# Performance work log

Hardware: AMD Instinct MI355X
Metric: run time of the kernel (lower is better)

Reference implementation:

```python
import jax, jax.numpy as jnp
import numpy as np
from math import factorial

# ---- static configuration (matches init_kwargs) ----
IRREPS_IN1 = [(32, 0, 1), (32, 1, -1), (32, 2, 1)]   # (mul, l, parity)
IRREPS_SH  = [(1, 0, 1), (1, 1, -1), (1, 2, 1)]
IRREPS_OUT = [(32, 0, 1), (32, 1, -1), (32, 2, 1)]
NUM_BASIS = 10
HIDDEN = 16
CUTOFF = 4.0
P_ENV = 6  # dimenet envelope_exponent (5) + 1

# ---- real Wigner 3j (Clebsch-Gordan in real SH basis), computed once in numpy ----
def _su2_cg(j1, j2, j3, m1, m2, m3):
    if m3 != m1 + m2:
        return 0.0
    f = factorial
    vmin = max(-j1 + j2 + m3, -j1 + m1, 0)
    vmax = min(j2 + j3 + m1, j3 - j1 + j2, j3 + m3)
    c = (f(2*j3+1) * f(j3+j1-j2) * f(j3-j1+j2) * f(j1+j2-j3) / f(j1+j2+j3+1)
         * f(j3+m3) * f(j3-m3) / (f(j1+m1) * f(j1-m1) * f(j2+m2) * f(j2-m2))) ** 0.5
    s = 0.0
    for v in range(vmin, vmax + 1):
        s += (-1)**(v + j2 + m2) * f(j2+j3+m1-v) * f(j1-m1+v) / (
             f(v) * f(j3-j1+j2-v) * f(j3+m3-v) * f(v+j1-j2-m3))
    return c * s

def _q(l):  # real -> complex SH change of basis
    q = np.zeros((2*l+1, 2*l+1), dtype=complex)
    for m in range(-l, 0):
        q[l+m, l+abs(m)] = 2**-0.5
        q[l+m, l-abs(m)] = -1j * 2**-0.5
    q[l, l] = 1.0
    for m in range(1, l+1):
        q[l+m, l+abs(m)] = (-1)**m * 2**-0.5
        q[l+m, l-abs(m)] = 1j * (-1)**m * 2**-0.5
    return (-1j)**l * q

def _wigner_3j(l1, l2, l3):
    csu2 = np.array([[[ _su2_cg(l1, l2, l3, m1, m2, m3)
                       for m3 in range(-l3, l3+1)]
                      for m2 in range(-l2, l2+1)]
                     for m1 in range(-l1, l1+1)], dtype=complex)
    c = np.einsum('ij,kl,mn,ikm->jln', _q(l1), _q(l2), np.conj(_q(l3)), csu2)
    c = np.real(c)
    n = np.linalg.norm(c)
    return c / n if n > 0 else c

def _slices(irreps):
    s, off = [], 0
    for mul, l, p in irreps:
        d = mul * (2*l + 1)
        s.append((off, off + d))
        off += d
    return s, off

SL1, DIM_IN1 = _slices(IRREPS_IN1)
SL2, DIM_SH = _slices(IRREPS_SH)
SL3, DIM_OUT = _slices(IRREPS_OUT)

_raw = []
for i1, (m1, l1, p1) in enumerate(IRREPS_IN1):
    for i2, (m2, l2, p2) in enumerate(IRREPS_SH):
        for i3, (m3, l3, p3) in enumerate(IRREPS_OUT):
            if p1 * p2 == p3 and abs(l1 - l2) <= l3 <= l1 + l2:
                _raw.append((i1, i2, i3))

_fan = {}
for i1, i2, i3 in _raw:  # path_normalization='element': fan-in per output slot
    _fan[i3] = _fan.get(i3, 0) + IRREPS_IN1[i1][0] * IRREPS_SH[i2][0]

INSTR = []
WEIGHT_NUMEL = 0
for i1, i2, i3 in _raw:
    m1, l1, _ = IRREPS_IN1[i1]
    m2, l2, _ = IRREPS_SH[i2]
    m3, l3, _ = IRREPS_OUT[i3]
    pw = ((2*l3 + 1) / _fan[i3]) ** 0.5  # irrep_normalization='component'
    C = _wigner_3j(l1, l2, l3).astype(np.float32)
    INSTR.append((i1, i2, i3, m1, l1, m2, l2, m3, l3, WEIGHT_NUMEL, pw, C))
    WEIGHT_NUMEL += m1 * m2 * m3

# ---- radial network: Bessel basis (with dimenet envelope) -> Linear -> SiLU -> Linear ----
def _radial(distance, freq, W1, b1, W2, b2):
    d = distance[:, 0]                      # squeeze(-1) -> [E]
    x = (d / CUTOFF)[:, None]               # [E, 1]
    p = P_ENV
    a = -(p + 1) * (p + 2) / 2.0
    b = float(p * (p + 2))
    c = -p * (p + 1) / 2.0
    env = (1.0 / x + a * x**(p-1) + b * x**p + c * x**(p+1)) * (x < 1.0).astype(x.dtype)
    basis = env * jnp.sin(freq * x)         # [E, NUM_BASIS]
    h = jax.nn.silu(basis @ W1 + b1)
    return h @ W2 + b2                      # [E, WEIGHT_NUMEL]

# ---- fully connected tensor product (uvw, external per-edge weights) ----
def _tp(x, sh, weights):
    E = x.shape[0]
    acc = [jnp.zeros((E, m, 2*l + 1), x.dtype) for m, l, _ in IRREPS_OUT]
    for (i1, i2, i3, m1, l1, m2, l2, m3, l3, woff, pw, C) in INSTR:
        a, b = SL1[i1]; xb = x[:, a:b].reshape(E, m1, 2*l1 + 1)
        a, b = SL2[i2]; sb = sh[:, a:b].reshape(E, m2, 2*l2 + 1)
        w = weights[:, woff:woff + m1*m2*m3].reshape(E, m1, m2, m3)
        Cj = jnp.asarray(C)
        acc[i3] = acc[i3] + pw * jnp.einsum('euvw,ijk,eui,evj->ewk', w, Cj, xb, sb)
    return jnp.concatenate([a.reshape(E, -1) for a in acc], axis=1)


def setup_inputs() -> dict:
    key = jax.random.key(0)
    ks = jax.random.split(key, 6)
    E = 16384
    x = jax.random.normal(ks[0], (E, DIM_IN1), jnp.float32)
    rel_pos_sh = jax.random.normal(ks[1], (E, DIM_SH), jnp.float32)
    # distances strictly inside (0, cutoff) so envelope 1/x and mask are benign
    distance = 0.25 + 3.5 * jax.random.uniform(ks[2], (E, 1), jnp.float32)
    freq = jnp.pi * jnp.arange(1, NUM_BASIS + 1, dtype=jnp.float32)
    W1 = 0.4 * jax.random.normal(ks[3], (NUM_BASIS, HIDDEN), jnp.float32)
    b1 = jnp.zeros((HIDDEN,), jnp.float32)
    W2 = 0.1 * jax.random.normal(ks[4], (HIDDEN, WEIGHT_NUMEL), jnp.float32)
    b2 = jnp.zeros((WEIGHT_NUMEL,), jnp.float32)
    return {"x": x, "rel_pos_sh": rel_pos_sh, "distance": distance,
            "freq": freq, "W1": W1, "b1": b1, "W2": W2, "b2": b2}


def reference(x, rel_pos_sh, distance, freq, W1, b1, W2, b2):
    weights = _radial(distance, freq, W1, b1, W2, b2)
    return _tp(x, rel_pos_sh, weights)
```

## Files before the change

kernel.cpp:

```cpp
#include <hip/hip_runtime.h>
#include <cmath>
#include <complex>
#include <cstring>
#include <algorithm>

#define DIM_IN  288
#define DIM_SHD 9
#define NB      10
#define NH      16
#define EPB     16
#define BLOCK   256
#define NINSTR  11
#define XSTR    292
#define ZG_STRIDE 116
#define ZG_SIZE  (16 * ZG_STRIDE)
#define W2B_ELEMS (NINSTR * 32 * 32 * 32)

#define OFF_SH 7424
#define POOLSZ 7616

typedef __attribute__((ext_vector_type(8))) short  short8b;
typedef __attribute__((ext_vector_type(4))) float  f32x4;
typedef __attribute__((ext_vector_type(2))) float  f32x2;

__device__ float g_C[NINSTR][125];

__device__ __forceinline__ unsigned short f2bf(float f) {
  unsigned int u = __float_as_uint(f);
  unsigned int r = (u + 0x7fffu + ((u >> 16) & 1u)) >> 16;
  return (unsigned short)r;
}

__global__ __launch_bounds__(256) void prep_w2(const float* __restrict__ W2,
                                               const float* __restrict__ b2,
                                               unsigned short* __restrict__ W2b) {
  int gid = blockIdx.x * 256 + threadIdx.x;
  if (gid < W2B_ELEMS) {
    int c = gid >> 5, t = gid & 31;
    float v = (t < 16) ? W2[(size_t)t * 11264 + c] : (t == 16 ? b2[c] : 0.0f);
    W2b[gid] = f2bf(v);
  }
}

template<int INS,int D1,int D2,int D3,int OFF2,int SLOT>
__device__ __forceinline__ void z_one(const float (&xv)[D1],
                                      const float* __restrict__ she,
                                      float* __restrict__ zo)
{
  const float* __restrict__ Cp = g_C[INS];
  constexpr int NP = D3 / 2;
  f32x2 zk2[NP > 0 ? NP : 1];
  float zkl = 0.f;
  #pragma unroll
  for (int m = 0; m < NP; ++m) zk2[m] = (f32x2){0.f, 0.f};
  #pragma unroll
  for (int i = 0; i < D1; ++i) {
    #pragma unroll
    for (int j = 0; j < D2; ++j) {
      float pr = xv[i] * she[OFF2 + j];
      f32x2 pr2 = {pr, pr};
      const float* cb = Cp + (i * D2 + j) * D3;
      #pragma unroll
      for (int m = 0; m < NP; ++m) {
        f32x2 cc = {cb[2 * m], cb[2 * m + 1]};
        zk2[m] = __builtin_elementwise_fma(cc, pr2, zk2[m]);
      }
      zkl = fmaf(cb[D3 - 1], pr, zkl);
    }
  }
  #pragma unroll
  for (int m = 0; m < NP; ++m) {
    zo[(SLOT + 2 * m) * 8]     = zk2[m].x;
    zo[(SLOT + 2 * m + 1) * 8] = zk2[m].y;
  }
  zo[(SLOT + D3 - 1) * 8] = zkl;
}

template<int D1,int OFF1>
__device__ __forceinline__ void load_x(const float* __restrict__ xg, int e0,
                                       int e, int u, float (&xv)[D1]) {
  const float* xp = xg + (size_t)(e0 + e) * DIM_IN + OFF1 + u * D1;
  #pragma unroll
  for (int i = 0; i < D1; ++i) xv[i] = xp[i];
}

__device__ __forceinline__ void z_group_l0(int lane, int q, int e0,
    const float* __restrict__ xg, const float* __restrict__ s_sh,
    float* __restrict__ zw) {
  #pragma unroll
  for (int s = 0; s < 2; ++s) {
    int id = lane + s * 64;
    int e = id >> 3, ul = id & 7, u = q * 8 + ul;
    float xv[1];
    load_x<1, 0>(xg, e0, e, u, xv);
    const float* she = s_sh + e * 12;
    float* zo = zw + e * ZG_STRIDE + ul;
    z_one<0, 1, 1, 1, 0, 0>(xv, she, zo);
    z_one<1, 1, 3, 3, 1, 1>(xv, she, zo);
    z_one<2, 1, 5, 5, 4, 4>(xv, she, zo);
  }
}

__device__ __forceinline__ void z_group_l1(int lane, int q, int e0,
    const float* __restrict__ xg, const float* __restrict__ s_sh,
    float* __restrict__ zw) {
  #pragma unroll
  for (int s = 0; s < 2; ++s) {
    int id = lane + s * 64;
    int e = id >> 3, ul = id & 7, u = q * 8 + ul;
    float xv[3];
    load_x<3, 32>(xg, e0, e, u, xv);
    const float* she = s_sh + e * 12;
    float* zo = zw + e * ZG_STRIDE + ul;
    z_one<3, 3, 1, 3, 0, 0>(xv, she, zo);
    z_one<4, 3, 3, 1, 1, 3>(xv, she, zo);
    z_one<5, 3, 3, 5, 1, 4>(xv, she, zo);
    z_one<6, 3, 5, 3, 4, 9>(xv, she, zo);
  }
}

__device__ __forceinline__ void z_group_l2(int lane, int q, int e0,
    const float* __restrict__ xg, const float* __restrict__ s_sh,
    float* __restrict__ zw) {
  #pragma unroll
  for (int s = 0; s < 2; ++s) {
    int id = lane + s * 64;
    int e = id >> 3, ul = id & 7, u = q * 8 + ul;
    float xv[5];
    load_x<5, 128>(xg, e0, e, u, xv);
    const float* she = s_sh + e * 12;
    float* zo = zw + e * ZG_STRIDE + ul;
    z_one< 7, 5, 1, 5, 0, 0>(xv, she, zo);
    z_one< 8, 5, 3, 3, 1, 5>(xv, she, zo);
    z_one< 9, 5, 5, 1, 4, 8>(xv, she, zo);
    z_one<10, 5, 5, 5, 4, 9>(xv, she, zo);
  }
}

template<int INS,int D3,int SB,int SLOT>
__device__ __forceinline__ void contract_q(
    int ls, int lq, int q,
    const unsigned short* __restrict__ W2b,
    const float* __restrict__ zw, short8b hB, f32x2 (&acc)[2][2][9])
{
  const unsigned short* Ap =
      W2b + ((size_t)(INS * 32 + q * 8) * 32 + ls) * 32 + lq * 8;
  const float* zb = zw + ls * ZG_STRIDE + SLOT * 8;
  const f32x4 zero4 = {0.f, 0.f, 0.f, 0.f};

  short8b R0c = *(const short8b*)(Ap);
  short8b R1c = *(const short8b*)(Ap + 512);
  short8b R0n = *(const short8b*)(Ap + 1024);
  short8b R1n = *(const short8b*)(Ap + 1536);
  f32x4 w0_cur = __builtin_amdgcn_mfma_f32_16x16x32_bf16(R0c, hB, zero4, 0, 0, 0);
  f32x4 w1_cur = __builtin_amdgcn_mfma_f32_16x16x32_bf16(R1c, hB, zero4, 0, 0, 0);

  #pragma unroll
  for (int c = 0; c < 2; ++c) {
    float4 zq[D3];
    #pragma unroll
    for (int k = 0; k < D3; ++k)
      zq[k] = *(const float4*)(zb + k * 8 + c * 4);
    #pragma unroll
    for (int i = 0; i < 4; ++i) {
      const int g = c * 4 + i;
      f32x4 w0n, w1n;
      if (g < 7) {
        w0n = __builtin_amdgcn_mfma_f32_16x16x32_bf16(R0n, hB, zero4, 0, 0, 0);
        w1n = __builtin_amdgcn_mfma_f32_16x16x32_bf16(R1n, hB, zero4, 0, 0, 0);
        if (g + 2 < 8) {
          R0n = *(const short8b*)(Ap + (size_t)(g + 2) * 1024);
          R1n = *(const short8b*)(Ap + (size_t)(g + 2) * 1024 + 512);
        }
      }
      f32x2 w0lo = {w0_cur[0], w0_cur[1]};
      f32x2 w0hi = {w0_cur[2], w0_cur[3]};
      f32x2 w1lo = {w1_cur[0], w1_cur[1]};
      f32x2 w1hi = {w1_cur[2], w1_cur[3]};
      #pragma unroll
      for (int k = 0; k < D3; ++k) {
        const float zz = (i == 0) ? zq[k].x : (i == 1) ? zq[k].y
                       : (i == 2) ? zq[k].z : zq[k].w;
        f32x2 zv = {zz, zz};
        acc[0][0][SB + k] = __builtin_elementwise_fma(w0lo, zv, acc[0][0][SB + k]);
        acc[0][1][SB + k] = __builtin_elementwise_fma(w0hi, zv, acc[0][1][SB + k]);
        acc[1][0][SB + k] = __builtin_elementwise_fma(w1lo, zv, acc[1][0][SB + k]);
        acc[1][1][SB + k] = __builtin_elementwise_fma(w1hi, zv, acc[1][1][SB + k]);
      }
      if (g < 7) { w0_cur = w0n; w1_cur = w1n; }
    }
  }
}

__global__ __launch_bounds__(BLOCK, 2) void conv_kernel(
    const float* __restrict__ xg, const float* __restrict__ shg,
    const float* __restrict__ dist, const float* __restrict__ freq,
    const float* __restrict__ W1, const float* __restrict__ b1,
    const unsigned short* __restrict__ W2b,
    float* __restrict__ out)
{
  __shared__ float s_pool[POOLSZ];
  float* s_sh = s_pool + OFF_SH;

  const int tid = threadIdx.x;
  const int e0 = blockIdx.x * EPB;
  const int lane = tid & 63;
  const int ls = lane & 15;
  const int lq = lane >> 4;
  const int q   = tid >> 6;
  float* zw = s_pool + q * ZG_SIZE;
  float* s_basis = s_pool + 2 * ZG_SIZE;
  unsigned short* s_hb = (unsigned short*)(s_pool + 3 * ZG_SIZE);

  if (tid < EPB * DIM_SHD) {
    int e = tid / DIM_SHD, c = tid - (tid / DIM_SHD) * DIM_SHD;
    s_sh[e * 12 + c] = shg[(size_t)(e0 + e) * DIM_SHD + c];
  }
  if (tid < EPB * NB) {
    int e = tid / NB, n = tid - (tid / NB) * NB;
    float d  = dist[e0 + e];
    float xv = d * 0.25f;
    float x2 = xv * xv, x4 = x2 * x2, x5 = x4 * xv;
    float env = 1.0f / xv + x5 * fmaf(xv, fmaf(xv, -21.0f, 48.0f), -28.0f);
    env = (xv < 1.0f) ? env : 0.0f;
    s_basis[e * NB + n] = env * sinf(freq[n] * xv);
  }
  __syncthreads();

  {
    int e = tid >> 4, t = tid & 15;
    float v = b1[t];
    #pragma unroll
    for (int n = 0; n < NB; ++n) v = fmaf(s_basis[e * NB + n], W1[n * NH + t], v);
    v = v / (1.0f + expf(-v));
    s_hb[e * 32 + t] = f2bf(v);
    s_hb[e * 32 + t + 16] = (t == 0) ? (unsigned short)0x3F80 : (unsigned short)0;
  }
  __syncthreads();
  short8b hB = *(const short8b*)(s_hb + ls * 32 + lq * 8);
  __syncthreads();

  f32x2 acc[2][2][9];
  #pragma unroll
  for (int wt = 0; wt < 2; ++wt)
    #pragma unroll
    for (int p = 0; p < 2; ++p)
      #pragma unroll
      for (int a = 0; a < 9; ++a) acc[wt][p][a] = (f32x2){0.f, 0.f};

  z_group_l0(lane, q, e0, xg, s_sh, zw);
  contract_q< 0, 1, 0, 0>(ls, lq, q, W2b, zw, hB, acc);
  contract_q< 1, 3, 1, 1>(ls, lq, q, W2b, zw, hB, acc);
  contract_q< 2, 5, 4, 4>(ls, lq, q, W2b, zw, hB, acc);

  z_group_l1(lane, q, e0, xg, s_sh, zw);
  contract_q< 3, 3, 1, 0>(ls, lq, q, W2b, zw, hB, acc);
  contract_q< 4, 1, 0, 3>(ls, lq, q, W2b, zw, hB, acc);
  contract_q< 5, 5, 4, 4>(ls, lq, q, W2b, zw, hB, acc);
  contract_q< 6, 3, 1, 9>(ls, lq, q, W2b, zw, hB, acc);

  z_group_l2(lane, q, e0, xg, s_sh, zw);
  contract_q< 7, 5, 4, 0>(ls, lq, q, W2b, zw, hB, acc);
  contract_q< 8, 3, 1, 5>(ls, lq, q, W2b, zw, hB, acc);
  contract_q< 9, 1, 0, 8>(ls, lq, q, W2b, zw, hB, acc);
  contract_q<10, 5, 4, 9>(ls, lq, q, W2b, zw, hB, acc);

  __syncthreads();
  float* s_og = s_pool;
  #pragma unroll
  for (int ph = 3; ph >= 0; --ph) {
    if (q == ph) {
      float* row = s_og + ls * XSTR;
      #pragma unroll
      for (int wt = 0; wt < 2; ++wt) {
        #pragma unroll
        for (int r = 0; r < 4; ++r) {
          const int w = wt * 16 + lq * 4 + r;
          float vals[9];
          #pragma unroll
          for (int a = 0; a < 9; ++a)
            vals[a] = (r & 1) ? acc[wt][r >> 1][a].y : acc[wt][r >> 1][a].x;
          if (ph == 3) {
            row[w] = vals[0];
            #pragma unroll
            for (int k = 0; k < 3; ++k) row[32 + w * 3 + k] = vals[1 + k];
            #pragma unroll
            for (int k = 0; k < 5; ++k) row[128 + w * 5 + k] = vals[4 + k];
          } else {
            row[w] += vals[0];
            #pragma unroll
            for (int k = 0; k < 3; ++k) row[32 + w * 3 + k] += vals[1 + k];
            #pragma unroll
            for (int k = 0; k < 5; ++k) row[128 + w * 5 + k] += vals[4 + k];
          }
        }
      }
    }
    __syncthreads();
  }
  for (int i4 = tid; i4 < EPB * 72; i4 += BLOCK) {
    int e = i4 / 72, r = i4 - e * 72;
    float4 v = *(const float4*)(s_og + e * XSTR + r * 4);
    *(float4*)(out + (size_t)(e0 + e) * DIM_IN + r * 4) = v;
  }
}

typedef std::complex<double> cd;

static double factd(int n) { double r = 1; for (int i = 2; i <= n; ++i) r *= i; return r; }

static double su2_cg(int j1, int j2, int j3, int m1, int m2, int m3) {
  if (m3 != m1 + m2) return 0.0;
  int vmin = std::max(std::max(-j1 + j2 + m3, -j1 + m1), 0);
  int vmax = std::min(std::min(j2 + j3 + m1, j3 - j1 + j2), j3 + m3);
  if (vmax < vmin) return 0.0;
  double c = std::sqrt(
      factd(2*j3+1) * factd(j3+j1-j2) * factd(j3-j1+j2) * factd(j1+j2-j3) / factd(j1+j2+j3+1)
      * factd(j3+m3) * factd(j3-m3)
      / (factd(j1+m1) * factd(j1-m1) * factd(j2+m2) * factd(j2-m2)));
  double s = 0.0;
  for (int v = vmin; v <= vmax; ++v) {
    double sg = ((v + j2 + m2) & 1) ? -1.0 : 1.0;
    s += sg * factd(j2+j3+m1-v) * factd(j1-m1+v)
         / (factd(v) * factd(j3-j1+j2-v) * factd(j3+m3-v) * factd(v+j1-j2-m3));
  }
  return c * s;
}

static void qmat(int l, cd q[5][5]) {
  for (int a = 0; a < 5; ++a) for (int b = 0; b < 5; ++b) q[a][b] = cd(0, 0);
  const double s = 1.0 / std::sqrt(2.0);
  for (int m = -l; m < 0; ++m) {
    q[l + m][l - m] = cd(s, 0);
    q[l + m][l + m] = cd(0, -s);
  }
  q[l][l] = cd(1, 0);
  for (int m = 1; m <= l; ++m) {
    double sg = (m & 1) ? -1.0 : 1.0;
    q[l + m][l + m] = cd(sg * s, 0);
    q[l + m][l - m] = cd(0, sg * s);
  }
  cd ph = (l == 0) ? cd(1, 0) : (l == 1) ? cd(0, -1) : cd(-1, 0);
  for (int a = 0; a < 5; ++a) for (int b = 0; b < 5; ++b) q[a][b] *= ph;
}

static void wigner3j(int l1, int l2, int l3, double C[5][5][5]) {
  int d1 = 2*l1+1, d2 = 2*l2+1, d3 = 2*l3+1;
  cd q1[5][5], q2[5][5], q3[5][5];
  qmat(l1, q1); qmat(l2, q2); qmat(l3, q3);
  double norm2 = 0;
  for (int j = 0; j < d1; ++j)
    for (int l = 0; l < d2; ++l)
      for (int n = 0; n < d3; ++n) {
        cd sum(0, 0);
        for (int i = 0; i < d1; ++i)
          for (int k = 0; k < d2; ++k)
            for (int m = 0; m < d3; ++m) {
              double cg = su2_cg(l1, l2, l3, i - l1, k - l2, m - l3);
              if (cg != 0.0) sum += q1[i][j] * q2[k][l] * std::conj(q3[m][n]) * cg;
            }
        C[j][l][n] = sum.real();
        norm2 += C[j][l][n] * C[j][l][n];
      }
  double nrm = std::sqrt(norm2);
  if (nrm > 0)
    for (int j = 0; j < d1; ++j)
      for (int l = 0; l < d2; ++l)
        for (int n = 0; n < d3; ++n) C[j][l][n] /= nrm;
}

static void build_C_host(float C_out[NINSTR][125]) {
  const int L1[NINSTR] = {0,0,0,1,1,1,1,2,2,2,2};
  const int L2[NINSTR] = {0,1,2,0,1,1,2,0,1,2,2};
  const int L3[NINSTR] = {0,1,2,1,0,2,1,2,1,0,2};
  std::memset(C_out, 0, sizeof(float) * NINSTR * 125);
  for (int ins = 0; ins < NINSTR; ++ins) {
    int l1 = L1[ins], l2 = L2[ins], l3 = L3[ins];
    int d1 = 2*l1+1, d2 = 2*l2+1, d3 = 2*l3+1;
    double C[5][5][5];
    wigner3j(l1, l2, l3, C);
    double fan = (l3 == 0) ? 96.0 : 128.0;
    double pw = std::sqrt((2*l3+1) / fan);
    for (int i = 0; i < d1; ++i)
      for (int j = 0; j < d2; ++j)
        for (int k = 0; k < d3; ++k)
          C_out[ins][(i * d2 + j) * d3 + k] = (float)(pw * C[i][j][k]);
  }
}

extern "C" void kernel_launch(void* const* d_in, const int* in_sizes, int n_in,
                              void* d_out, int out_size, void* d_ws, size_t ws_size,
                              hipStream_t stream) {
  static float hC[NINSTR][125];
  build_C_host(hC);
  void* dC = nullptr;
  hipGetSymbolAddress(&dC, HIP_SYMBOL(g_C));
  hipMemcpyAsync(dC, hC, sizeof(hC), hipMemcpyHostToDevice, stream);

  const float* xg   = (const float*)d_in[0];
  const float* shg  = (const float*)d_in[1];
  const float* dist = (const float*)d_in[2];
  const float* freq = (const float*)d_in[3];
  const float* W1   = (const float*)d_in[4];
  const float* b1   = (const float*)d_in[5];
  const float* W2   = (const float*)d_in[6];
  const float* b2   = (const float*)d_in[7];
  float* out = (float*)d_out;
  unsigned short* W2b = (unsigned short*)d_ws;

  prep_w2<<<(W2B_ELEMS + 255) / 256, 256, 0, stream>>>(W2, b2, W2b);

  int E = in_sizes[2];
  int blocks = E / EPB;
  conv_kernel<<<blocks, BLOCK, 0, stream>>>(xg, shg, dist, freq, W1, b1, W2b, out);
}
```

Before: 68.27 us.

## Split u-dimension across eight waves per block instead of four

```diff
diff --git a/kernel.cpp b/kernel.cpp
--- a/kernel.cpp
+++ b/kernel.cpp
@@ -9,11 +9,11 @@
 #define NB      10
 #define NH      16
 #define EPB     16
-#define BLOCK   256
+#define BLOCK   512
 #define NINSTR  11
 #define XSTR    292
-#define ZG_STRIDE 116
-#define ZG_SIZE  (16 * ZG_STRIDE)
+#define ZW_STRIDE 58
+#define ZW_SIZE  (16 * ZW_STRIDE)
 #define W2B_ELEMS (NINSTR * 32 * 32 * 32)
 
 #define OFF_SH 7424
@@ -70,10 +70,10 @@
   }
   #pragma unroll
   for (int m = 0; m < NP; ++m) {
-    zo[(SLOT + 2 * m) * 8]     = zk2[m].x;
-    zo[(SLOT + 2 * m + 1) * 8] = zk2[m].y;
-  }
-  zo[(SLOT + D3 - 1) * 8] = zkl;
+    zo[(SLOT + 2 * m) * 4]     = zk2[m].x;
+    zo[(SLOT + 2 * m + 1) * 4] = zk2[m].y;
+  }
+  zo[(SLOT + D3 - 1) * 4] = zkl;
 }
 
 template<int D1,int OFF1>
@@ -84,110 +84,88 @@
   for (int i = 0; i < D1; ++i) xv[i] = xp[i];
 }
 
-__device__ __forceinline__ void z_group_l0(int lane, int q, int e0,
+__device__ __forceinline__ void z_group_l0(int lane, int q8, int e0,
     const float* __restrict__ xg, const float* __restrict__ s_sh,
     float* __restrict__ zw) {
-  #pragma unroll
-  for (int s = 0; s < 2; ++s) {
-    int id = lane + s * 64;
-    int e = id >> 3, ul = id & 7, u = q * 8 + ul;
-    float xv[1];
-    load_x<1, 0>(xg, e0, e, u, xv);
-    const float* she = s_sh + e * 12;
-    float* zo = zw + e * ZG_STRIDE + ul;
-    z_one<0, 1, 1, 1, 0, 0>(xv, she, zo);
-    z_one<1, 1, 3, 3, 1, 1>(xv, she, zo);
-    z_one<2, 1, 5, 5, 4, 4>(xv, she, zo);
-  }
-}
-
-__device__ __forceinline__ void z_group_l1(int lane, int q, int e0,
+  int e = lane >> 2, ul = lane & 3, u = q8 * 4 + ul;
+  float xv[1];
+  load_x<1, 0>(xg, e0, e, u, xv);
+  const float* she = s_sh + e * 12;
+  float* zo = zw + e * ZW_STRIDE + ul;
+  z_one<0, 1, 1, 1, 0, 0>(xv, she, zo);
+  z_one<1, 1, 3, 3, 1, 1>(xv, she, zo);
+  z_one<2, 1, 5, 5, 4, 4>(xv, she, zo);
+}
+
+__device__ __forceinline__ void z_group_l1(int lane, int q8, int e0,
     const float* __restrict__ xg, const float* __restrict__ s_sh,
     float* __restrict__ zw) {
-  #pragma unroll
-  for (int s = 0; s < 2; ++s) {
-    int id = lane + s * 64;
-    int e = id >> 3, ul = id & 7, u = q * 8 + ul;
-    float xv[3];
-    load_x<3, 32>(xg, e0, e, u, xv);
-    const float* she = s_sh + e * 12;
-    float* zo = zw + e * ZG_STRIDE + ul;
-    z_one<3, 3, 1, 3, 0, 0>(xv, she, zo);
-    z_one<4, 3, 3, 1, 1, 3>(xv, she, zo);
-    z_one<5, 3, 3, 5, 1, 4>(xv, she, zo);
-    z_one<6, 3, 5, 3, 4, 9>(xv, she, zo);
-  }
-}
-
-__device__ __forceinline__ void z_group_l2(int lane, int q, int e0,
+  int e = lane >> 2, ul = lane & 3, u = q8 * 4 + ul;
+  float xv[3];
+  load_x<3, 32>(xg, e0, e, u, xv);
+  const float* she = s_sh + e * 12;
+  float* zo = zw + e * ZW_STRIDE + ul;
+  z_one<3, 3, 1, 3, 0, 0>(xv, she, zo);
+  z_one<4, 3, 3, 1, 1, 3>(xv, she, zo);
+  z_one<5, 3, 3, 5, 1, 4>(xv, she, zo);
+  z_one<6, 3, 5, 3, 4, 9>(xv, she, zo);
+}
+
+__device__ __forceinline__ void z_group_l2(int lane, int q8, int e0,
     const float* __restrict__ xg, const float* __restrict__ s_sh,
     float* __restrict__ zw) {
-  #pragma unroll
-  for (int s = 0; s < 2; ++s) {
-    int id = lane + s * 64;
-    int e = id >> 3, ul = id & 7, u = q * 8 + ul;
-    float xv[5];
-    load_x<5, 128>(xg, e0, e, u, xv);
-    const float* she = s_sh + e * 12;
-    float* zo = zw + e * ZG_STRIDE + ul;
-    z_one< 7, 5, 1, 5, 0, 0>(xv, she, zo);
-    z_one< 8, 5, 3, 3, 1, 5>(xv, she, zo);
-    z_one< 9, 5, 5, 1, 4, 8>(xv, she, zo);
-    z_one<10, 5, 5, 5, 4, 9>(xv, she, zo);
-  }
+  int e = lane >> 2, ul = lane & 3, u = q8 * 4 + ul;
+  float xv[5];
+  load_x<5, 128>(xg, e0, e, u, xv);
+  const float* she = s_sh + e * 12;
+  float* zo = zw + e * ZW_STRIDE + ul;
+  z_one< 7, 5, 1, 5, 0, 0>(xv, she, zo);
+  z_one< 8, 5, 3, 3, 1, 5>(xv, she, zo);
+  z_one< 9, 5, 5, 1, 4, 8>(xv, she, zo);
+  z_one<10, 5, 5, 5, 4, 9>(xv, she, zo);
 }
 
 template<int INS,int D3,int SB,int SLOT>
-__device__ __forceinline__ void contract_q(
-    int ls, int lq, int q,
+__device__ __forceinline__ void contract8(
+    int ls, int lq, int q8,
     const unsigned short* __restrict__ W2b,
     const float* __restrict__ zw, short8b hB, f32x2 (&acc)[2][2][9])
 {
   const unsigned short* Ap =
-      W2b + ((size_t)(INS * 32 + q * 8) * 32 + ls) * 32 + lq * 8;
-  const float* zb = zw + ls * ZG_STRIDE + SLOT * 8;
+      W2b + ((size_t)(INS * 32 + q8 * 4) * 32 + ls) * 32 + lq * 8;
+  const float* zb = zw + ls * ZW_STRIDE + SLOT * 4;
   const f32x4 zero4 = {0.f, 0.f, 0.f, 0.f};
 
-  short8b R0c = *(const short8b*)(Ap);
-  short8b R1c = *(const short8b*)(Ap + 512);
-  short8b R0n = *(const short8b*)(Ap + 1024);
-  short8b R1n = *(const short8b*)(Ap + 1536);
-  f32x4 w0_cur = __builtin_amdgcn_mfma_f32_16x16x32_bf16(R0c, hB, zero4, 0, 0, 0);
-  f32x4 w1_cur = __builtin_amdgcn_mfma_f32_16x16x32_bf16(R1c, hB, zero4, 0, 0, 0);
-
-  #pragma unroll
-  for (int c = 0; c < 2; ++c) {
-    float4 zq[D3];
+  #pragma unroll
+  for (int wt = 0; wt < 2; ++wt) {
+    const unsigned short* Aw = Ap + wt * 512;
+    short8b A0 = *(const short8b*)(Aw);
+    short8b A1 = *(const short8b*)(Aw + 1024);
+    short8b A2 = *(const short8b*)(Aw + 2048);
+    short8b A3 = *(const short8b*)(Aw + 3072);
+    f32x4 w_cur = __builtin_amdgcn_mfma_f32_16x16x32_bf16(A0, hB, zero4, 0, 0, 0);
+    f32x2 zp[D3];
     #pragma unroll
-    for (int k = 0; k < D3; ++k)
-      zq[k] = *(const float4*)(zb + k * 8 + c * 4);
-    #pragma unroll
-    for (int i = 0; i < 4; ++i) {
-      const int g = c * 4 + i;
-      f32x4 w0n, w1n;
-      if (g < 7) {
-        w0n = __builtin_amdgcn_mfma_f32_16x16x32_bf16(R0n, hB, zero4, 0, 0, 0);
-        w1n = __builtin_amdgcn_mfma_f32_16x16x32_bf16(R1n, hB, zero4, 0, 0, 0);
-        if (g + 2 < 8) {
-          R0n = *(const short8b*)(Ap + (size_t)(g + 2) * 1024);
-          R1n = *(const short8b*)(Ap + (size_t)(g + 2) * 1024 + 512);
-        }
-      }
-      f32x2 w0lo = {w0_cur[0], w0_cur[1]};
-      f32x2 w0hi = {w0_cur[2], w0_cur[3]};
-      f32x2 w1lo = {w1_cur[0], w1_cur[1]};
-      f32x2 w1hi = {w1_cur[2], w1_cur[3]};
+    for (int g = 0; g < 4; ++g) {
+      f32x4 w_next;
+      if (g == 0) w_next = __builtin_amdgcn_mfma_f32_16x16x32_bf16(A1, hB, zero4, 0, 0, 0);
+      if (g == 1) w_next = __builtin_amdgcn_mfma_f32_16x16x32_bf16(A2, hB, zero4, 0, 0, 0);
+      if (g == 2) w_next = __builtin_amdgcn_mfma_f32_16x16x32_bf16(A3, hB, zero4, 0, 0, 0);
+      if ((g & 1) == 0) {
+        #pragma unroll
+        for (int k = 0; k < D3; ++k)
+          zp[k] = *(const f32x2*)(zb + k * 4 + g);
+      }
+      f32x2 wlo = {w_cur[0], w_cur[1]};
+      f32x2 whi = {w_cur[2], w_cur[3]};
       #pragma unroll
       for (int k = 0; k < D3; ++k) {
-        const float zz = (i == 0) ? zq[k].x : (i == 1) ? zq[k].y
-                       : (i == 2) ? zq[k].z : zq[k].w;
+        const float zz = (g & 1) ? zp[k].y : zp[k].x;
         f32x2 zv = {zz, zz};
-        acc[0][0][SB + k] = __builtin_elementwise_fma(w0lo, zv, acc[0][0][SB + k]);
-        acc[0][1][SB + k] = __builtin_elementwise_fma(w0hi, zv, acc[0][1][SB + k]);
-        acc[1][0][SB + k] = __builtin_elementwise_fma(w1lo, zv, acc[1][0][SB + k]);
-        acc[1][1][SB + k] = __builtin_elementwise_fma(w1hi, zv, acc[1][1][SB + k]);
-      }
-      if (g < 7) { w0_cur = w0n; w1_cur = w1n; }
+        acc[wt][0][SB + k] = __builtin_elementwise_fma(wlo, zv, acc[wt][0][SB + k]);
+        acc[wt][1][SB + k] = __builtin_elementwise_fma(whi, zv, acc[wt][1][SB + k]);
+      }
+      if (g < 3) w_cur = w_next;
     }
   }
 }
@@ -207,10 +185,10 @@
   const int lane = tid & 63;
   const int ls = lane & 15;
   const int lq = lane >> 4;
-  const int q   = tid >> 6;
-  float* zw = s_pool + q * ZG_SIZE;
-  float* s_basis = s_pool + 2 * ZG_SIZE;
-  unsigned short* s_hb = (unsigned short*)(s_pool + 3 * ZG_SIZE);
+  const int q8  = tid >> 6;
+  float* zw = s_pool + q8 * ZW_SIZE;
+  float* s_basis = s_pool + 6 * ZW_SIZE;
+  unsigned short* s_hb = (unsigned short*)(s_pool + 7 * ZW_SIZE);
 
   if (tid < EPB * DIM_SHD) {
     int e = tid / DIM_SHD, c = tid - (tid / DIM_SHD) * DIM_SHD;
@@ -227,7 +205,7 @@
   }
   __syncthreads();
 
-  {
+  if (tid < EPB * NH) {
     int e = tid >> 4, t = tid & 15;
     float v = b1[t];
     #pragma unroll
@@ -248,28 +226,28 @@
       #pragma unroll
       for (int a = 0; a < 9; ++a) acc[wt][p][a] = (f32x2){0.f, 0.f};
 
-  z_group_l0(lane, q, e0, xg, s_sh, zw);
-  contract_q< 0, 1, 0, 0>(ls, lq, q, W2b, zw, hB, acc);
-  contract_q< 1, 3, 1, 1>(ls, lq, q, W2b, zw, hB, acc);
-  contract_q< 2, 5, 4, 4>(ls, lq, q, W2b, zw, hB, acc);
-
-  z_group_l1(lane, q, e0, xg, s_sh, zw);
-  contract_q< 3, 3, 1, 0>(ls, lq, q, W2b, zw, hB, acc);
-  contract_q< 4, 1, 0, 3>(ls, lq, q, W2b, zw, hB, acc);
-  contract_q< 5, 5, 4, 4>(ls, lq, q, W2b, zw, hB, acc);
-  contract_q< 6, 3, 1, 9>(ls, lq, q, W2b, zw, hB, acc);
-
-  z_group_l2(lane, q, e0, xg, s_sh, zw);
-  contract_q< 7, 5, 4, 0>(ls, lq, q, W2b, zw, hB, acc);
-  contract_q< 8, 3, 1, 5>(ls, lq, q, W2b, zw, hB, acc);
-  contract_q< 9, 1, 0, 8>(ls, lq, q, W2b, zw, hB, acc);
-  contract_q<10, 5, 4, 9>(ls, lq, q, W2b, zw, hB, acc);
+  z_group_l0(lane, q8, e0, xg, s_sh, zw);
+  contract8< 0, 1, 0, 0>(ls, lq, q8, W2b, zw, hB, acc);
+  contract8< 1, 3, 1, 1>(ls, lq, q8, W2b, zw, hB, acc);
+  contract8< 2, 5, 4, 4>(ls, lq, q8, W2b, zw, hB, acc);
+
+  z_group_l1(lane, q8, e0, xg, s_sh, zw);
+  contract8< 3, 3, 1, 0>(ls, lq, q8, W2b, zw, hB, acc);
+  contract8< 4, 1, 0, 3>(ls, lq, q8, W2b, zw, hB, acc);
+  contract8< 5, 5, 4, 4>(ls, lq, q8, W2b, zw, hB, acc);
+  contract8< 6, 3, 1, 9>(ls, lq, q8, W2b, zw, hB, acc);
+
+  z_group_l2(lane, q8, e0, xg, s_sh, zw);
+  contract8< 7, 5, 4, 0>(ls, lq, q8, W2b, zw, hB, acc);
+  contract8< 8, 3, 1, 5>(ls, lq, q8, W2b, zw, hB, acc);
+  contract8< 9, 1, 0, 8>(ls, lq, q8, W2b, zw, hB, acc);
+  contract8<10, 5, 4, 9>(ls, lq, q8, W2b, zw, hB, acc);
 
   __syncthreads();
   float* s_og = s_pool;
   #pragma unroll
-  for (int ph = 3; ph >= 0; --ph) {
-    if (q == ph) {
+  for (int ph = 7; ph >= 0; --ph) {
+    if (q8 == ph) {
       float* row = s_og + ls * XSTR;
       #pragma unroll
       for (int wt = 0; wt < 2; ++wt) {
@@ -280,7 +258,7 @@
           #pragma unroll
           for (int a = 0; a < 9; ++a)
             vals[a] = (r & 1) ? acc[wt][r >> 1][a].y : acc[wt][r >> 1][a].x;
-          if (ph == 3) {
+          if (ph == 7) {
             row[w] = vals[0];
             #pragma unroll
             for (int k = 0; k < 3; ++k) row[32 + w * 3 + k] = vals[1 + k];
```

Result: slower. 102.7 us (+50.5%).

## Split output-channel halves into two sequential passes to halve accumulator registers

Applied to the files above, without the earlier changes.

```diff
diff --git a/kernel.cpp b/kernel.cpp
--- a/kernel.cpp
+++ b/kernel.cpp
@@ -137,23 +137,20 @@
   }
 }
 
-template<int INS,int D3,int SB,int SLOT>
-__device__ __forceinline__ void contract_q(
+template<int INS,int D3,int SB,int SLOT,int WT>
+__device__ __forceinline__ void contract_h(
     int ls, int lq, int q,
     const unsigned short* __restrict__ W2b,
-    const float* __restrict__ zw, short8b hB, f32x2 (&acc)[2][2][9])
+    const float* __restrict__ zw, short8b hB, f32x2 (&acc)[2][9])
 {
   const unsigned short* Ap =
-      W2b + ((size_t)(INS * 32 + q * 8) * 32 + ls) * 32 + lq * 8;
+      W2b + ((size_t)(INS * 32 + q * 8) * 32 + ls) * 32 + lq * 8 + WT * 512;
   const float* zb = zw + ls * ZG_STRIDE + SLOT * 8;
   const f32x4 zero4 = {0.f, 0.f, 0.f, 0.f};
 
-  short8b R0c = *(const short8b*)(Ap);
-  short8b R1c = *(const short8b*)(Ap + 512);
-  short8b R0n = *(const short8b*)(Ap + 1024);
-  short8b R1n = *(const short8b*)(Ap + 1536);
-  f32x4 w0_cur = __builtin_amdgcn_mfma_f32_16x16x32_bf16(R0c, hB, zero4, 0, 0, 0);
-  f32x4 w1_cur = __builtin_amdgcn_mfma_f32_16x16x32_bf16(R1c, hB, zero4, 0, 0, 0);
+  short8b Rc = *(const short8b*)(Ap);
+  short8b Rn = *(const short8b*)(Ap + 1024);
+  f32x4 w_cur = __builtin_amdgcn_mfma_f32_16x16x32_bf16(Rc, hB, zero4, 0, 0, 0);
 
   #pragma unroll
   for (int c = 0; c < 2; ++c) {
@@ -164,32 +161,96 @@
     #pragma unroll
     for (int i = 0; i < 4; ++i) {
       const int g = c * 4 + i;
-      f32x4 w0n, w1n;
+      f32x4 w_next;
       if (g < 7) {
-        w0n = __builtin_amdgcn_mfma_f32_16x16x32_bf16(R0n, hB, zero4, 0, 0, 0);
-        w1n = __builtin_amdgcn_mfma_f32_16x16x32_bf16(R1n, hB, zero4, 0, 0, 0);
-        if (g + 2 < 8) {
-          R0n = *(const short8b*)(Ap + (size_t)(g + 2) * 1024);
-          R1n = *(const short8b*)(Ap + (size_t)(g + 2) * 1024 + 512);
-        }
+        w_next = __builtin_amdgcn_mfma_f32_16x16x32_bf16(Rn, hB, zero4, 0, 0, 0);
+        if (g + 2 < 8) Rn = *(const short8b*)(Ap + (size_t)(g + 2) * 1024);
       }
-      f32x2 w0lo = {w0_cur[0], w0_cur[1]};
-      f32x2 w0hi = {w0_cur[2], w0_cur[3]};
-      f32x2 w1lo = {w1_cur[0], w1_cur[1]};
-      f32x2 w1hi = {w1_cur[2], w1_cur[3]};
+      f32x2 wlo = {w_cur[0], w_cur[1]};
+      f32x2 whi = {w_cur[2], w_cur[3]};
       #pragma unroll
       for (int k = 0; k < D3; ++k) {
         const float zz = (i == 0) ? zq[k].x : (i == 1) ? zq[k].y
                        : (i == 2) ? zq[k].z : zq[k].w;
         f32x2 zv = {zz, zz};
-        acc[0][0][SB + k] = __builtin_elementwise_fma(w0lo, zv, acc[0][0][SB + k]);
-        acc[0][1][SB + k] = __builtin_elementwise_fma(w0hi, zv, acc[0][1][SB + k]);
-        acc[1][0][SB + k] = __builtin_elementwise_fma(w1lo, zv, acc[1][0][SB + k]);
-        acc[1][1][SB + k] = __builtin_elementwise_fma(w1hi, zv, acc[1][1][SB + k]);
+        acc[0][SB + k] = __builtin_elementwise_fma(wlo, zv, acc[0][SB + k]);
+        acc[1][SB + k] = __builtin_elementwise_fma(whi, zv, acc[1][SB + k]);
       }
-      if (g < 7) { w0_cur = w0n; w1_cur = w1n; }
+      if (g < 7) w_cur = w_next;
     }
   }
+}
+
+template<int WT>
+__device__ __forceinline__ void run_pass(
+    int tid, int lane, int ls, int lq, int q, int e0,
+    const float* __restrict__ xg, const float* __restrict__ s_sh,
+    float* __restrict__ zw, float* __restrict__ s_pool,
+    const unsigned short* __restrict__ W2b, short8b hB,
+    float* __restrict__ out)
+{
+  f32x2 acc[2][9];
+  #pragma unroll
+  for (int p = 0; p < 2; ++p)
+    #pragma unroll
+    for (int a = 0; a < 9; ++a) acc[p][a] = (f32x2){0.f, 0.f};
+
+  z_group_l0(lane, q, e0, xg, s_sh, zw);
+  contract_h< 0, 1, 0, 0, WT>(ls, lq, q, W2b, zw, hB, acc);
+  contract_h< 1, 3, 1, 1, WT>(ls, lq, q, W2b, zw, hB, acc);
+  contract_h< 2, 5, 4, 4, WT>(ls, lq, q, W2b, zw, hB, acc);
+
+  z_group_l1(lane, q, e0, xg, s_sh, zw);
+  contract_h< 3, 3, 1, 0, WT>(ls, lq, q, W2b, zw, hB, acc);
+  contract_h< 4, 1, 0, 3, WT>(ls, lq, q, W2b, zw, hB, acc);
+  contract_h< 5, 5, 4, 4, WT>(ls, lq, q, W2b, zw, hB, acc);
+  contract_h< 6, 3, 1, 9, WT>(ls, lq, q, W2b, zw, hB, acc);
+
+  z_group_l2(lane, q, e0, xg, s_sh, zw);
+  contract_h< 7, 5, 4, 0, WT>(ls, lq, q, W2b, zw, hB, acc);
+  contract_h< 8, 3, 1, 5, WT>(ls, lq, q, W2b, zw, hB, acc);
+  contract_h< 9, 1, 0, 8, WT>(ls, lq, q, W2b, zw, hB, acc);
+  contract_h<10, 5, 4, 9, WT>(ls, lq, q, W2b, zw, hB, acc);
+
+  __syncthreads();
+  float* s_og = s_pool;
+  #pragma unroll
+  for (int ph = 3; ph >= 0; --ph) {
+    if (q == ph) {
+      float* row = s_og + ls * XSTR;
+      #pragma unroll
+      for (int r = 0; r < 4; ++r) {
+        const int w = WT * 16 + lq * 4 + r;
+        float vals[9];
+        #pragma unroll
+        for (int a = 0; a < 9; ++a)
+          vals[a] = (r & 1) ? acc[r >> 1][a].y : acc[r >> 1][a].x;
+        if (ph == 3) {
+          row[w] = vals[0];
+          #pragma unroll
+          for (int k = 0; k < 3; ++k) row[32 + w * 3 + k] = vals[1 + k];
+          #pragma unroll
+          for (int k = 0; k < 5; ++k) row[128 + w * 5 + k] = vals[4 + k];
+        } else {
+          row[w] += vals[0];
+          #pragma unroll
+          for (int k = 0; k < 3; ++k) row[32 + w * 3 + k] += vals[1 + k];
+          #pragma unroll
+          for (int k = 0; k < 5; ++k) row[128 + w * 5 + k] += vals[4 + k];
+        }
+      }
+    }
+    __syncthreads();
+  }
+  for (int i4 = tid; i4 < EPB * 36; i4 += BLOCK) {
+    int e = i4 / 36, r = i4 - e * 36;
+    int col = (r < 4)  ? (WT * 16 + r * 4)
+            : (r < 16) ? (32 + WT * 48 + (r - 4) * 4)
+                       : (128 + WT * 80 + (r - 16) * 4);
+    float4 v = *(const float4*)(s_og + e * XSTR + col);
+    *(float4*)(out + (size_t)(e0 + e) * DIM_IN + col) = v;
+  }
+  __syncthreads();
 }
 
 __global__ __launch_bounds__(BLOCK, 2) void conv_kernel(
@@ -240,69 +301,8 @@
   short8b hB = *(const short8b*)(s_hb + ls * 32 + lq * 8);
   __syncthreads();
 
-  f32x2 acc[2][2][9];
-  #pragma unroll
-  for (int wt = 0; wt < 2; ++wt)
-    #pragma unroll
-    for (int p = 0; p < 2; ++p)
-      #pragma unroll
-      for (int a = 0; a < 9; ++a) acc[wt][p][a] = (f32x2){0.f, 0.f};
-
-  z_group_l0(lane, q, e0, xg, s_sh, zw);
-  contract_q< 0, 1, 0, 0>(ls, lq, q, W2b, zw, hB, acc);
-  contract_q< 1, 3, 1, 1>(ls, lq, q, W2b, zw, hB, acc);
-  contract_q< 2, 5, 4, 4>(ls, lq, q, W2b, zw, hB, acc);
-
-  z_group_l1(lane, q, e0, xg, s_sh, zw);
-  contract_q< 3, 3, 1, 0>(ls, lq, q, W2b, zw, hB, acc);
-  contract_q< 4, 1, 0, 3>(ls, lq, q, W2b, zw, hB, acc);
-  contract_q< 5, 5, 4, 4>(ls, lq, q, W2b, zw, hB, acc);
-  contract_q< 6, 3, 1, 9>(ls, lq, q, W2b, zw, hB, acc);
-
-  z_group_l2(lane, q, e0, xg, s_sh, zw);
-  contract_q< 7, 5, 4, 0>(ls, lq, q, W2b, zw, hB, acc);
-  contract_q< 8, 3, 1, 5>(ls, lq, q, W2b, zw, hB, acc);
-  contract_q< 9, 1, 0, 8>(ls, lq, q, W2b, zw, hB, acc);
-  contract_q<10, 5, 4, 9>(ls, lq, q, W2b, zw, hB, acc);
-
-  __syncthreads();
-  float* s_og = s_pool;
-  #pragma unroll
-  for (int ph = 3; ph >= 0; --ph) {
-    if (q == ph) {
-      float* row = s_og + ls * XSTR;
-      #pragma unroll
-      for (int wt = 0; wt < 2; ++wt) {
-        #pragma unroll
-        for (int r = 0; r < 4; ++r) {
-          const int w = wt * 16 + lq * 4 + r;
-          float vals[9];
-          #pragma unroll
-          for (int a = 0; a < 9; ++a)
-            vals[a] = (r & 1) ? acc[wt][r >> 1][a].y : acc[wt][r >> 1][a].x;
-          if (ph == 3) {
-            row[w] = vals[0];
-            #pragma unroll
-            for (int k = 0; k < 3; ++k) row[32 + w * 3 + k] = vals[1 + k];
-            #pragma unroll
-            for (int k = 0; k < 5; ++k) row[128 + w * 5 + k] = vals[4 + k];
-          } else {
-            row[w] += vals[0];
-            #pragma unroll
-            for (int k = 0; k < 3; ++k) row[32 + w * 3 + k] += vals[1 + k];
-            #pragma unroll
-            for (int k = 0; k < 5; ++k) row[128 + w * 5 + k] += vals[4 + k];
-          }
-        }
-      }
-    }
-    __syncthreads();
-  }
-  for (int i4 = tid; i4 < EPB * 72; i4 += BLOCK) {
-    int e = i4 / 72, r = i4 - e * 72;
-    float4 v = *(const float4*)(s_og + e * XSTR + r * 4);
-    *(float4*)(out + (size_t)(e0 + e) * DIM_IN + r * 4) = v;
-  }
+  run_pass<0>(tid, lane, ls, lq, q, e0, xg, s_sh, zw, s_pool, W2b, hB, out);
+  run_pass<1>(tid, lane, ls, lq, q, e0, xg, s_sh, zw, s_pool, W2b, hB, out);
 }
 
 typedef std::complex<double> cd;
```

New measurement: 73.09 us. +7.1%, slower.
